# Performance work log

Measured on AMD Instinct MI355X. Metric: run time of the kernel, lower is better.

The kernel has to match this reference:

```python
import jax, jax.numpy as jnp
import numpy as np
import math

B, IN_CH, IMG = 32, 3, 128
D, L, H, MLP, P = 512, 8, 8, 2048, 8
HD = D // H
EPS = 1e-5


def _conv(x, w, b, stride, pad):
    y = jax.lax.conv_general_dilated(x, w, (stride, stride), pad,
                                     dimension_numbers=("NCHW", "OIHW", "NCHW"))
    return y + b[None, :, None, None]


def _gn(x, g, b, groups):
    Bn, C, Hh, W = x.shape
    xr = x.reshape(Bn, groups, C // groups, Hh, W)
    m = jnp.mean(xr, axis=(2, 3, 4), keepdims=True)
    v = jnp.var(xr, axis=(2, 3, 4), keepdims=True)
    xr = (xr - m) / jnp.sqrt(v + EPS)
    return xr.reshape(Bn, C, Hh, W) * g[None, :, None, None] + b[None, :, None, None]


def _ln(x, g, b):
    m = jnp.mean(x, axis=-1, keepdims=True)
    v = jnp.var(x, axis=-1, keepdims=True)
    return (x - m) / jnp.sqrt(v + EPS) * g + b


def _rot_half(x):
    # interleaved pairs: (x0,x1) -> (-x1,x0)
    x1, x2 = x[..., 0::2], x[..., 1::2]
    return jnp.stack((-x2, x1), axis=-1).reshape(x.shape)


def _xpos_tables(n_pos, hd):
    # faithful to rotary_embedding_torch with use_xpos=True, scale_base=512
    inv = 1.0 / (10000.0 ** (jnp.arange(0, hd, 2, dtype=jnp.float32) / hd))
    seq = jnp.arange(n_pos, dtype=jnp.float32)
    freqs = jnp.repeat(seq[:, None] * inv[None, :], 2, axis=-1)  # (n_pos, hd) interleaved
    sv = (jnp.arange(0, hd, 2, dtype=jnp.float32) + 0.4 * hd) / (1.4 * hd)
    power = (seq - n_pos // 2) / 512.0
    scale = sv[None, :] ** power[:, None]                        # (n_pos, hd//2)
    scale = jnp.concatenate([scale, scale], axis=-1)             # library uses cat, not interleave
    return jnp.cos(freqs), jnp.sin(freqs), scale


def _pos2d(N, Dd):
    g = int(math.isqrt(N))
    y = jnp.tile(jnp.arange(g), g).astype(jnp.float32)
    x = jnp.repeat(jnp.arange(g), g).astype(jnp.float32)
    dq = Dd // 4
    omega = jnp.exp(jnp.arange(dq, dtype=jnp.float32) * -(math.log(10000.0) / dq))
    px, py = x[:, None] * omega, y[:, None] * omega
    return jnp.concatenate([jnp.sin(px), jnp.cos(px), jnp.sin(py), jnp.cos(py)], axis=-1)[None]


def setup_inputs() -> dict:
    key = jax.random.key(0)
    ks = iter(jax.random.split(key, 40))
    def rn(shape, s=0.02):
        return jax.random.normal(next(ks), shape, jnp.float32) * s
    return dict(
        x=jax.random.normal(next(ks), (B, IN_CH, IMG, IMG), jnp.float32),
        conv1_w=rn((32, 3, 3, 3)), conv1_b=jnp.zeros((32,), jnp.float32),
        gn1_g=jnp.ones((32,), jnp.float32), gn1_b=jnp.zeros((32,), jnp.float32),
        conv2_w=rn((64, 32, 3, 3)), conv2_b=jnp.zeros((64,), jnp.float32),
        gn2_g=jnp.ones((64,), jnp.float32), gn2_b=jnp.zeros((64,), jnp.float32),
        patch_w=rn((D, 64, P, P)), patch_b=jnp.zeros((D,), jnp.float32),
        cls_token=rn((1, 1, D), 1.0),
        ln1_g=jnp.ones((L, D), jnp.float32), ln1_b=jnp.zeros((L, D), jnp.float32),
        qkv_w=rn((L, D, 3 * D)), qkv_b=jnp.zeros((L, 3 * D), jnp.float32),
        out_w=rn((L, D, D)), out_b=jnp.zeros((L, D), jnp.float32),
        ln2_g=jnp.ones((L, D), jnp.float32), ln2_b=jnp.zeros((L, D), jnp.float32),
        w1_w=rn((L, D, MLP)), w1_b=jnp.zeros((L, MLP), jnp.float32),
        w2_w=rn((L, D, MLP)), w2_b=jnp.zeros((L, MLP), jnp.float32),
        w3_w=rn((L, MLP, D)), w3_b=jnp.zeros((L, D), jnp.float32),
        fn_g=jnp.ones((D,), jnp.float32), fn_b=jnp.zeros((D,), jnp.float32),
    )


def _forward(x, conv1_w, conv1_b, gn1_g, gn1_b, conv2_w, conv2_b, gn2_g, gn2_b,
             patch_w, patch_b, cls_token, ln1_g, ln1_b, qkv_w, qkv_b, out_w, out_b,
             ln2_g, ln2_b, w1_w, w1_b, w2_w, w2_b, w3_w, w3_b, fn_g, fn_b):
    # conv stem (no downsample)
    f = jax.nn.gelu(_gn(_conv(x, conv1_w, conv1_b, 1, [(1, 1), (1, 1)]), gn1_g, gn1_b, 4), approximate=False)
    f = jax.nn.gelu(_gn(_conv(f, conv2_w, conv2_b, 1, [(1, 1), (1, 1)]), gn2_g, gn2_b, 8), approximate=False)
    # patch embed
    p = _conv(f, patch_w, patch_b, P, "VALID")            # (B, D, g, g)
    Bn, Dd, gh, gw = p.shape
    tokens = p.reshape(Bn, Dd, gh * gw).transpose(0, 2, 1)  # (B, N, D)
    tokens = tokens + _pos2d(gh * gw, Dd)
    xa = jnp.concatenate([jnp.broadcast_to(cls_token, (Bn, 1, Dd)), tokens], axis=1)
    # NOTE: original code applies RoPE with seq_dim=-2 on (B,S,H,hd) -> rotation indexed by HEAD axis
    cos, sin, xsc = _xpos_tables(H, HD)
    scale_att = HD ** -0.5
    for i in range(L):
        n = _ln(xa, ln1_g[i], ln1_b[i])
        qkv = (n @ qkv_w[i] + qkv_b[i]).reshape(Bn, -1, 3, H, HD)
        q, k, v = qkv[:, :, 0], qkv[:, :, 1], qkv[:, :, 2]     # (B, S, H, hd)
        q = q * cos * xsc + _rot_half(q) * sin * xsc
        k = k * cos / xsc + _rot_half(k) * sin / xsc
        attn = jax.nn.softmax(jnp.einsum("bihd,bjhd->bhij", q, k) * scale_att, axis=-1)
        y = jnp.einsum("bhij,bjhd->bihd", attn, v).reshape(Bn, -1, Dd)
        xa = xa + y @ out_w[i] + out_b[i]
        n2 = _ln(xa, ln2_g[i], ln2_b[i])
        xa = xa + (jax.nn.silu(n2 @ w1_w[i] + w1_b[i]) * (n2 @ w2_w[i] + w2_b[i])) @ w3_w[i] + w3_b[i]
    return _ln(xa, fn_g, fn_b)


def reference(x, conv1_w, conv1_b, gn1_g, gn1_b, conv2_w, conv2_b, gn2_g, gn2_b,
              patch_w, patch_b, cls_token, ln1_g, ln1_b, qkv_w, qkv_b, out_w, out_b,
              ln2_g, ln2_b, w1_w, w1_b, w2_w, w2_b, w3_w, w3_b, fn_g, fn_b):
    xa = _forward(x, conv1_w, conv1_b, gn1_g, gn1_b, conv2_w, conv2_b, gn2_g, gn2_b,
                  patch_w, patch_b, cls_token, ln1_g, ln1_b, qkv_w, qkv_b, out_w, out_b,
                  ln2_g, ln2_b, w1_w, w1_b, w2_w, w2_b, w3_w, w3_b, fn_g, fn_b)
    return (xa[:, 0], xa[:, 1:])  # (cls, patches); grid_hw is static (16,16)
```

## Files before the change

### kernel.cpp

```cpp
#include <hip/hip_runtime.h>

#define EPSV 1e-5f
typedef unsigned short u16;
typedef short bf16x8 __attribute__((ext_vector_type(8)));
typedef float f32x4 __attribute__((ext_vector_type(4)));
typedef u16 u16x8 __attribute__((ext_vector_type(8)));

__device__ __forceinline__ float gelu_exact(float x) {
    return 0.5f * x * (1.0f + erff(x * 0.7071067811865475f));
}
__device__ __forceinline__ u16 to_bf(float x) {
    union { float f; unsigned u; } c; c.f = x;
    unsigned r = c.u + 0x7fffu + ((c.u >> 16) & 1u);
    return (u16)(r >> 16);
}
__device__ __forceinline__ float to_f(u16 h) {
    union { unsigned u; float f; } c; c.u = ((unsigned)h) << 16;
    return c.f;
}
__device__ __forceinline__ void gload_lds16(const void* g, void* l) {
    __builtin_amdgcn_global_load_lds((const __attribute__((address_space(1))) unsigned int*)g,
                                     (__attribute__((address_space(3))) unsigned int*)l, 16, 0, 0);
}

__global__ void k_wsfail(float* out) { out[0] = 1.0e9f; }

__global__ void k_setup(float* __restrict__ sacc,
                        const float* __restrict__ conv1_w, float* __restrict__ w1t,
                        const float* __restrict__ conv2_w, u16* __restrict__ wpack,
                        const float* __restrict__ b1, const float* __restrict__ b2,
                        float* __restrict__ bias12,
                        float* __restrict__ postab, float* __restrict__ ropetab,
                        const float* __restrict__ cls, float* __restrict__ xa) {
    int idx = blockIdx.x * 256 + threadIdx.x;
    if (idx < 131072) {
        int p = idx >> 9, j = idx & 511;
        float coord = (j < 256) ? (float)(p >> 4) : (float)(p & 15);
        int jm = j & 127;
        float om = powf(10000.0f, -(float)jm / 128.0f);
        float arg = coord * om;
        postab[idx] = ((j >> 7) & 1) ? cosf(arg) : sinf(arg);
    }
    if (idx < 512) {
        int h = idx >> 6, d = idx & 63;
        float freq = (float)h * powf(10000.0f, -(float)(d >> 1) / 32.0f);
        float sv = (2.0f * (float)(d & 31) + 25.6f) / 89.6f;
        float pw = ((float)h - 4.0f) / 512.0f;
        float sc = powf(sv, pw);
        ropetab[idx * 4 + 0] = cosf(freq);
        ropetab[idx * 4 + 1] = sinf(freq);
        ropetab[idx * 4 + 2] = sc * 0.125f;
        ropetab[idx * 4 + 3] = 1.0f / sc;
    }
    if (idx < 768) sacc[idx] = 0.0f;
    if (idx < 864) {
        int co = idx / 27, k = idx % 27;
        w1t[k * 32 + co] = conv1_w[idx];
    }
    if (idx < 18432) {
        int ci = idx & 31, tc = idx >> 5;
        int tap = tc >> 6, co = tc & 63;
        wpack[idx] = to_bf(conv2_w[co * 288 + ci * 9 + tap]);
    }
    if (idx < 32768) {
        int l = idx >> 12, pc = idx & 4095;
        int chunk = pc >> 4, within = pc & 15;
        int srccol = (chunk >> 1) * 16 + within;
        bias12[idx] = (chunk & 1) ? b2[l * 2048 + srccol] : b1[l * 2048 + srccol];
    }
    if (idx < 16384) {
        int b = idx >> 9, d = idx & 511;
        xa[(size_t)(b * 257) * 512 + d] = cls[d];
    }
}

__global__ void k_pperm(const float* __restrict__ w, u16* __restrict__ wp) {
    int idx = blockIdx.x * 256 + threadIdx.x;
    int cout = idx >> 12, rem = idx & 4095;
    int tap = rem >> 6, ci = rem & 63;
    wp[idx] = to_bf(w[cout * 4096 + ci * 64 + tap]);
}

__global__ __launch_bounds__(256) void k_wcvtT(const float* __restrict__ src,
                                               u16* __restrict__ dst, int K, int N) {
    __shared__ float s[32][33];
    int z = blockIdx.z;
    src += (size_t)z * K * N;
    dst += (size_t)z * K * N;
    int k0 = blockIdx.y * 32, n0 = blockIdx.x * 32;
    int t = threadIdx.x, r = t >> 3, c4 = (t & 7) * 4;
    float4 v = *(const float4*)&src[(size_t)(k0 + r) * N + n0 + c4];
    s[r][c4 + 0] = v.x; s[r][c4 + 1] = v.y; s[r][c4 + 2] = v.z; s[r][c4 + 3] = v.w;
    __syncthreads();
    ushort4 o;
    o.x = to_bf(s[c4 + 0][r]); o.y = to_bf(s[c4 + 1][r]);
    o.z = to_bf(s[c4 + 2][r]); o.w = to_bf(s[c4 + 3][r]);
    *(ushort4*)&dst[(size_t)(n0 + r) * K + k0 + c4] = o;
}

__global__ __launch_bounds__(256) void k_wcvtT12L(const float* __restrict__ w1,
                                                  const float* __restrict__ w2,
                                                  u16* __restrict__ w12All) {
    __shared__ float s[32][33];
    int z = blockIdx.z;
    int layer = z >> 1, sel = z & 1;
    const float* src = (sel ? w2 : w1) + (size_t)layer * 1048576;
    u16* dst = w12All + (size_t)layer * 2097152;
    int k0 = blockIdx.y * 32, n0 = blockIdx.x * 32;
    int t = threadIdx.x, r = t >> 3, c4 = (t & 7) * 4;
    float4 v = *(const float4*)&src[(size_t)(k0 + r) * 2048 + n0 + c4];
    s[r][c4 + 0] = v.x; s[r][c4 + 1] = v.y; s[r][c4 + 2] = v.z; s[r][c4 + 3] = v.w;
    __syncthreads();
    ushort4 o;
    o.x = to_bf(s[c4 + 0][r]); o.y = to_bf(s[c4 + 1][r]);
    o.z = to_bf(s[c4 + 2][r]); o.w = to_bf(s[c4 + 3][r]);
    int nsrc = n0 + r;
    int p = ((nsrc >> 4) << 5) + (sel << 4) + (nsrc & 15);
    *(ushort4*)&dst[(size_t)p * 512 + k0 + c4] = o;
}

__global__ __launch_bounds__(256) void k_conv1(const float* __restrict__ in,
                                               const float* __restrict__ wt,
                                               const float* __restrict__ bias,
                                               u16* __restrict__ f1n,
                                               float* __restrict__ sacc) {
    __shared__ float s_in[3][18][18];
    __shared__ float rs[4][4], rq[4][4];
    int b = blockIdx.y;
    int tile = blockIdx.x;
    int y0 = (tile >> 3) << 4;
    int x0 = (tile & 7) << 4;
    int tid = threadIdx.x;
    for (int idx = tid; idx < 972; idx += 256) {
        int ci = idx / 324, r = idx % 324;
        int ly = r / 18, lx = r % 18;
        int gy = y0 + ly - 1, gx = x0 + lx - 1;
        float v = 0.0f;
        if (gy >= 0 && gy < 128 && gx >= 0 && gx < 128)
            v = in[((size_t)(b * 3 + ci) * 128 + gy) * 128 + gx];
        s_in[ci][ly][lx] = v;
    }
    __syncthreads();
    int py = tid >> 4, px = tid & 15;
    float acc[32];
#pragma unroll
    for (int co = 0; co < 32; co++) acc[co] = bias[co];
#pragma unroll
    for (int ci = 0; ci < 3; ci++)
#pragma unroll
        for (int dy = 0; dy < 3; dy++)
#pragma unroll
            for (int dx = 0; dx < 3; dx++) {
                float v = s_in[ci][py + dy][px + dx];
                const float* wr = &wt[(ci * 9 + dy * 3 + dx) * 32];
#pragma unroll
                for (int co = 0; co < 32; co++)
                    acc[co] = fmaf(wr[co], v, acc[co]);
            }
    float s[4] = {0.f, 0.f, 0.f, 0.f}, q[4] = {0.f, 0.f, 0.f, 0.f};
    u16 ob[32];
#pragma unroll
    for (int co = 0; co < 32; co++) {
        u16 hv = to_bf(acc[co]);
        ob[co] = hv;
        float v = to_f(hv);
        s[co >> 3] += v;
        q[co >> 3] += v * v;
    }
    int oy = y0 + py, ox = x0 + px;
    u16* dst = f1n + ((size_t)(b * 16384 + oy * 128 + ox) << 5);
#pragma unroll
    for (int i = 0; i < 8; i++)
        *(ushort4*)(dst + i * 4) = make_ushort4(ob[i * 4], ob[i * 4 + 1], ob[i * 4 + 2], ob[i * 4 + 3]);
#pragma unroll
    for (int g = 0; g < 4; g++) {
#pragma unroll
        for (int off = 1; off < 64; off <<= 1) {
            s[g] += __shfl_xor(s[g], off);
            q[g] += __shfl_xor(q[g], off);
        }
    }
    int w = tid >> 6, lane = tid & 63;
    if (lane == 0)
#pragma unroll
        for (int g = 0; g < 4; g++) { rs[g][w] = s[g]; rq[g][w] = q[g]; }
    __syncthreads();
    if (tid < 4) {
        int g = tid;
        float S = rs[g][0] + rs[g][1] + rs[g][2] + rs[g][3];
        float Q = rq[g][0] + rq[g][1] + rq[g][2] + rq[g][3];
        atomicAdd(&sacc[(b * 4 + g) * 2], S);
        atomicAdd(&sacc[(b * 4 + g) * 2 + 1], Q);
    }
}

__global__ void k_gnap(u16* __restrict__ xio, const float* __restrict__ sacc,
                       const float* __restrict__ gg, const float* __restrict__ bb,
                       int cm, int sh, int gmul) {
    int idx = blockIdx.x * 256 + threadIdx.x;
    long e = (long)idx * 4;
    int c0 = (int)(e & cm);
    int b = (int)(e >> sh);
    int sid = b * gmul + (c0 >> 3);
    float m = sacc[2 * sid] * (1.0f / 131072.0f);
    float var = sacc[2 * sid + 1] * (1.0f / 131072.0f) - m * m;
    float r = rsqrtf(var + 1e-5f);
    ushort4 a = *(ushort4*)&xio[e];
    ushort4 o;
    o.x = to_bf(gelu_exact((to_f(a.x) - m) * r * gg[c0 + 0] + bb[c0 + 0]));
    o.y = to_bf(gelu_exact((to_f(a.y) - m) * r * gg[c0 + 1] + bb[c0 + 1]));
    o.z = to_bf(gelu_exact((to_f(a.z) - m) * r * gg[c0 + 2] + bb[c0 + 2]));
    o.w = to_bf(gelu_exact((to_f(a.w) - m) * r * gg[c0 + 3] + bb[c0 + 3]));
    *(ushort4*)&xio[e] = o;
}

__global__ __launch_bounds__(256) void k_conv2m(const u16* __restrict__ f1b,
                                                const u16* __restrict__ wp,
                                                const float* __restrict__ bias,
                                                u16* __restrict__ f2n,
                                                float* __restrict__ sacc) {
    __shared__ u16 st[256][72];
    __shared__ float rs[8][4], rq[8][4];
    int b = blockIdx.y;
    int tile = blockIdx.x;
    int y0 = (tile >> 3) << 4;
    int x0 = (tile & 7) << 4;
    int tid = threadIdx.x;
    int w = tid >> 6, lane = tid & 63;
    int l15 = lane & 15, l16 = lane >> 4;

    const u16* base = f1b + ((size_t)b << 19);

    f32x4 acc[4][4];
    f32x4 zf = {0.f, 0.f, 0.f, 0.f};
#pragma unroll
    for (int m = 0; m < 4; m++)
#pragma unroll
        for (int n = 0; n < 4; n++) acc[m][n] = zf;
    bf16x8 zb = {0, 0, 0, 0, 0, 0, 0, 0};

#pragma unroll
    for (int tap = 0; tap < 9; tap++) {
        int dy = tap / 3, dx = tap % 3;
        int gx = x0 + l15 + dx - 1;
        bf16x8 af[4], bk[4];
#pragma unroll
        for (int m = 0; m < 4; m++) {
            int gy = y0 + w * 4 + m + dy - 1;
            bool ok = (gy >= 0) && (gy < 128) && (gx >= 0) && (gx < 128);
            int pix = ok ? (gy * 128 + gx) : 0;
            bf16x8 v = *(const bf16x8*)(base + ((size_t)pix << 5) + l16 * 8);
            af[m] = ok ? v : zb;
        }
#pragma unroll
        for (int n = 0; n < 4; n++)
            bk[n] = *(const bf16x8*)&wp[(tap * 64 + n * 16 + l15) * 32 + l16 * 8];
#pragma unroll
        for (int m = 0; m < 4; m++)
#pragma unroll
            for (int n = 0; n < 4; n++)
                acc[m][n] = __builtin_amdgcn_mfma_f32_16x16x32_bf16(af[m], bk[n], acc[m][n], 0, 0, 0);
    }

#pragma unroll
    for (int n = 0; n < 4; n++) {
        int ch = n * 16 + l15;
        float bv = bias[ch];
#pragma unroll
        for (int m = 0; m < 4; m++) {
#pragma unroll
            for (int r = 0; r < 4; r++) {
                int lpix = (w * 4 + m) * 16 + l16 * 4 + r;
                st[lpix][ch] = to_bf(acc[m][n][r] + bv);
            }
        }
    }
    __syncthreads();

    int py = tid >> 4, pxx = tid & 15;
    u16* dstp = f2n + ((size_t)(b * 16384 + (y0 + py) * 128 + x0 + pxx) << 6);
    float gs[8], gq[8];
#pragma unroll
    for (int g = 0; g < 8; g++) { gs[g] = 0.0f; gq[g] = 0.0f; }
#pragma unroll
    for (int c0 = 0; c0 < 8; c0++) {
        u16x8 v = *(const u16x8*)&st[tid][c0 * 8];
        *(u16x8*)(dstp + c0 * 8) = v;
#pragma unroll
        for (int i = 0; i < 8; i++) {
            float f = to_f((u16)v[i]);
            gs[c0] += f;
            gq[c0] += f * f;
        }
    }
#pragma unroll
    for (int g = 0; g < 8; g++) {
#pragma unroll
        for (int off = 1; off < 64; off <<= 1) {
            gs[g] += __shfl_xor(gs[g], off);
            gq[g] += __shfl_xor(gq[g], off);
        }
    }
    if (lane == 0)
#pragma unroll
        for (int g = 0; g < 8; g++) { rs[g][w] = gs[g]; rq[g][w] = gq[g]; }
    __syncthreads();
    if (tid < 8) {
        int g = tid;
        float S = rs[g][0] + rs[g][1] + rs[g][2] + rs[g][3];
        float Q = rq[g][0] + rq[g][1] + rq[g][2] + rq[g][3];
        atomicAdd(&sacc[(b * 8 + g) * 2], S);
        atomicAdd(&sacc[(b * 8 + g) * 2 + 1], Q);
    }
}

template <int MODE, int EPI>
__global__ __launch_bounds__(256) void k_bgemm(const u16* __restrict__ A,
                                               const u16* __restrict__ Bt,
                                               const float* __restrict__ bias,
                                               void* __restrict__ Cp,
                                               const float* __restrict__ aux,
                                               int M, int N, int K) {
    __shared__ u16 ldsA[8192];
    __shared__ u16 ldsB[8192];
    int tid = threadIdx.x;
    int w = tid >> 6, lane = tid & 63;
    int bm = blockIdx.y * 128, bn = blockIdx.x * 128;
    int wr = w >> 1, wc = w & 1;
    int l15 = lane & 15, l16 = lane >> 4;

    f32x4 acc[4][4];
    f32x4 zf = {0.f, 0.f, 0.f, 0.f};
#pragma unroll
    for (int m = 0; m < 4; m++)
#pragma unroll
        for (int n = 0; n < 4; n++) acc[m][n] = zf;

    for (int k0 = 0; k0 < K; k0 += 64) {
#pragma unroll
        for (int i = 0; i < 4; i++) {
            int chunk = (w * 4 + i) * 64 + lane;
            int kg = chunk >> 7, row = chunk & 127;
            const u16* src;
            if (MODE == 0) {
                int grow = bm + row;
                if (grow > M - 1) grow = M - 1;
                src = A + (size_t)grow * K + k0 + kg * 8;
            } else {
                int grow = bm + row;
                int bimg = grow >> 8, p = grow & 255;
                int kga = (k0 >> 3) + kg;
                int tap = kga >> 3, cq = kga & 7;
                int ky = tap >> 3, kx = tap & 7;
                int gy = ((p >> 4) << 3) + ky, gx = ((p & 15) << 3) + kx;
                src = A + (((size_t)(bimg * 16384 + gy * 128 + gx)) << 6) + cq * 8;
            }
            gload_lds16(src, &ldsA[(w * 4 + i) * 512]);
        }
#pragma unroll
        for (int i = 0; i < 4; i++) {
            int chunk = (w * 4 + i) * 64 + lane;
            int col = chunk >> 3, kgs = chunk & 7;
            int kg_src = kgs ^ (col & 7);
            const u16* src = Bt + (size_t)(bn + col) * K + k0 + kg_src * 8;
            gload_lds16(src, &ldsB[(w * 4 + i) * 512]);
        }
        __syncthreads();

        bf16x8 af[4][2], bfr[4][2];
#pragma unroll
        for (int kk = 0; kk < 2; kk++) {
            int kga = kk * 4 + l16;
#pragma unroll
            for (int m = 0; m < 4; m++) {
                int row_l = wr * 64 + m * 16 + l15;
                af[m][kk] = *(const bf16x8*)&ldsA[(kga * 128 + row_l) * 8];
            }
#pragma unroll
            for (int n = 0; n < 4; n++) {
                int col_l = wc * 64 + n * 16 + l15;
                bfr[n][kk] = *(const bf16x8*)&ldsB[(col_l * 8 + (kga ^ (col_l & 7))) * 8];
            }
        }
#pragma unroll
        for (int m = 0; m < 4; m++)
#pragma unroll
            for (int n = 0; n < 4; n++) {
                acc[m][n] = __builtin_amdgcn_mfma_f32_16x16x32_bf16(af[m][0], bfr[n][0], acc[m][n], 0, 0, 0);
                acc[m][n] = __builtin_amdgcn_mfma_f32_16x16x32_bf16(af[m][1], bfr[n][1], acc[m][n], 0, 0, 0);
            }
        __syncthreads();
    }

    if (EPI == 6) {
#pragma unroll
        for (int np = 0; np < 2; np++) {
            int n_a = np * 2, n_b = np * 2 + 1;
            float bva = bias[bn + wc * 64 + n_a * 16 + l15];
            float bvb = bias[bn + wc * 64 + n_b * 16 + l15];
            int ocol = (bn >> 1) + wc * 32 + np * 16 + l15;
#pragma unroll
            for (int m = 0; m < 4; m++) {
#pragma unroll
                for (int r = 0; r < 4; r++) {
                    int grow = bm + wr * 64 + m * 16 + l16 * 4 + r;
                    if (grow < M) {
                        float h1v = to_f(to_bf(acc[m][n_a][r] + bva));
                        float h2v = to_f(to_bf(acc[m][n_b][r] + bvb));
                        float sl = h1v / (1.0f + __expf(-h1v));
                        ((u16*)Cp)[(size_t)grow * (N >> 1) + ocol] = to_bf(sl * h2v);
                    }
                }
            }
        }
    } else {
#pragma unroll
        for (int n = 0; n < 4; n++) {
            int gcol = bn + wc * 64 + n * 16 + l15;
            float bv = bias[gcol];
            float rc = 0.f, rsn = 0.f, rsc = 1.f;
            bool isqk = false, odd = false;
            if (EPI == 7) {
                isqk = gcol < 1024;
                odd = (l15 & 1) != 0;
                const float* rb = &aux[(gcol & 511) * 4];
                if (isqk) {
                    rc = rb[0]; rsn = rb[1];
                    rsc = (gcol < 512) ? rb[2] : rb[3];
                }
            }
#pragma unroll
            for (int m = 0; m < 4; m++) {
#pragma unroll
                for (int r = 0; r < 4; r++) {
                    int grow = bm + wr * 64 + m * 16 + l16 * 4 + r;
                    float v = acc[m][n][r] + bv;
                    if (EPI == 7) {
                        float p = __shfl_xor(v, 1);
                        float vr = isqk ? ((odd ? (v * rc + p * rsn) : (v * rc - p * rsn)) * rsc) : v;
                        if (grow < M) ((u16*)Cp)[(size_t)grow * N + gcol] = to_bf(vr);
                    } else if (EPI == 1) {
                        if (grow < M) ((float*)Cp)[(size_t)grow * N + gcol] = v;
                    } else if (EPI == 2) {
                        if (grow < M) ((float*)Cp)[(size_t)grow * N + gcol] += v;
                    } else {
                        int bimg = grow >> 8, p2 = grow & 255;
                        v += aux[p2 * 512 + gcol];
                        ((float*)Cp)[((size_t)(bimg * 257) + 1 + p2) * 512 + gcol] = v;
                    }
                }
            }
        }
    }
}

__global__ __launch_bounds__(256) void k_bgemm64(const u16* __restrict__ A,
                                                 const u16* __restrict__ Bt,
                                                 const float* __restrict__ bias,
                                                 float* __restrict__ C,
                                                 int M, int N, int K) {
    __shared__ u16 ldsA[4096];
    __shared__ u16 ldsB[8192];
    int tid = threadIdx.x;
    int w = tid >> 6, lane = tid & 63;
    int bm = blockIdx.y * 64, bn = blockIdx.x * 128;
    int l15 = lane & 15, l16 = lane >> 4;

    f32x4 acc[4][2];
    f32x4 zf = {0.f, 0.f, 0.f, 0.f};
#pragma unroll
    for (int m = 0; m < 4; m++)
#pragma unroll
        for (int n = 0; n < 2; n++) acc[m][n] = zf;

    for (int k0 = 0; k0 < K; k0 += 64) {
#pragma unroll
        for (int i = 0; i < 2; i++) {
            int chunk = (w * 2 + i) * 64 + lane;
            int kg = chunk >> 6, row = chunk & 63;
            int grow = bm + row;
            if (grow > M - 1) grow = M - 1;
            const u16* src = A + (size_t)grow * K + k0 + kg * 8;
            gload_lds16(src, &ldsA[(w * 2 + i) * 512]);
        }
#pragma unroll
        for (int i = 0; i < 4; i++) {
            int chunk = (w * 4 + i) * 64 + lane;
            int col = chunk >> 3, kgs = chunk & 7;
            int kg_src = kgs ^ (col & 7);
            const u16* src = Bt + (size_t)(bn + col) * K + k0 + kg_src * 8;
            gload_lds16(src, &ldsB[(w * 4 + i) * 512]);
        }
        __syncthreads();

        bf16x8 af[4][2], bfr[2][2];
#pragma unroll
        for (int kk = 0; kk < 2; kk++) {
            int kga = kk * 4 + l16;
#pragma unroll
            for (int m = 0; m < 4; m++) {
                int row_l = m * 16 + l15;
                af[m][kk] = *(const bf16x8*)&ldsA[(kga * 64 + row_l) * 8];
            }
#pragma unroll
            for (int n = 0; n < 2; n++) {
                int col_l = w * 32 + n * 16 + l15;
                bfr[n][kk] = *(const bf16x8*)&ldsB[(col_l * 8 + (kga ^ (col_l & 7))) * 8];
            }
        }
#pragma unroll
        for (int m = 0; m < 4; m++)
#pragma unroll
            for (int n = 0; n < 2; n++) {
                acc[m][n] = __builtin_amdgcn_mfma_f32_16x16x32_bf16(af[m][0], bfr[n][0], acc[m][n], 0, 0, 0);
                acc[m][n] = __builtin_amdgcn_mfma_f32_16x16x32_bf16(af[m][1], bfr[n][1], acc[m][n], 0, 0, 0);
            }
        __syncthreads();
    }

#pragma unroll
    for (int n = 0; n < 2; n++) {
        int gcol = bn + w * 32 + n * 16 + l15;
        float bv = bias[gcol];
#pragma unroll
        for (int m = 0; m < 4; m++) {
#pragma unroll
            for (int r = 0; r < 4; r++) {
                int grow = bm + m * 16 + l16 * 4 + r;
                if (grow < M) C[(size_t)grow * N + gcol] += acc[m][n][r] + bv;
            }
        }
    }
}

__global__ __launch_bounds__(256) void k_lnb(const float* __restrict__ x,
                                             const float* __restrict__ g,
                                             const float* __restrict__ bta,
                                             u16* __restrict__ o) {
    int row = blockIdx.x * 4 + (threadIdx.x >> 6);
    int lane = threadIdx.x & 63;
    const float4* xr = (const float4*)(x + (size_t)row * 512);
    float4 a = xr[lane * 2], b = xr[lane * 2 + 1];
    float s = a.x + a.y + a.z + a.w + b.x + b.y + b.z + b.w;
#pragma unroll
    for (int off = 1; off < 64; off <<= 1) s += __shfl_xor(s, off);
    float mean = s * (1.0f / 512.0f);
    float d[8] = {a.x - mean, a.y - mean, a.z - mean, a.w - mean,
                  b.x - mean, b.y - mean, b.z - mean, b.w - mean};
    float q = 0.0f;
#pragma unroll
    for (int i = 0; i < 8; i++) q += d[i] * d[i];
#pragma unroll
    for (int off = 1; off < 64; off <<= 1) q += __shfl_xor(q, off);
    float rstd = rsqrtf(q * (1.0f / 512.0f) + EPSV);
    int c0 = lane * 8;
    float4 g0 = *(const float4*)&g[c0], g1 = *(const float4*)&g[c0 + 4];
    float4 b0 = *(const float4*)&bta[c0], b1 = *(const float4*)&bta[c0 + 4];
    u16* orow = o + (size_t)row * 512 + c0;
    *(ushort4*)orow = make_ushort4(to_bf(d[0] * rstd * g0.x + b0.x), to_bf(d[1] * rstd * g0.y + b0.y),
                                   to_bf(d[2] * rstd * g0.z + b0.z), to_bf(d[3] * rstd * g0.w + b0.w));
    *(ushort4*)(orow + 4) = make_ushort4(to_bf(d[4] * rstd * g1.x + b1.x), to_bf(d[5] * rstd * g1.y + b1.y),
                                         to_bf(d[6] * rstd * g1.z + b1.z), to_bf(d[7] * rstd * g1.w + b1.w));
}

__global__ __launch_bounds__(256) void k_ln_out(const float* __restrict__ x,
                                                const float* __restrict__ g,
                                                const float* __restrict__ bta,
                                                float* __restrict__ out) {
    int row = blockIdx.x * 4 + (threadIdx.x >> 6);
    int lane = threadIdx.x & 63;
    const float4* xr = (const float4*)(x + (size_t)row * 512);
    float4 a = xr[lane * 2], b = xr[lane * 2 + 1];
    float s = a.x + a.y + a.z + a.w + b.x + b.y + b.z + b.w;
#pragma unroll
    for (int off = 1; off < 64; off <<= 1) s += __shfl_xor(s, off);
    float mean = s * (1.0f / 512.0f);
    float d[8] = {a.x - mean, a.y - mean, a.z - mean, a.w - mean,
                  b.x - mean, b.y - mean, b.z - mean, b.w - mean};
    float q = 0.0f;
#pragma unroll
    for (int i = 0; i < 8; i++) q += d[i] * d[i];
#pragma unroll
    for (int off = 1; off < 64; off <<= 1) q += __shfl_xor(q, off);
    float rstd = rsqrtf(q * (1.0f / 512.0f) + EPSV);
    int bb = row / 257, t = row % 257;
    float* dst = (t == 0) ? out + (size_t)bb * 512
                          : out + 16384 + (size_t)(bb * 256 + (t - 1)) * 512;
    int c0 = lane * 8;
    float4 g0 = *(const float4*)&g[c0], g1 = *(const float4*)&g[c0 + 4];
    float4 b0 = *(const float4*)&bta[c0], b1 = *(const float4*)&bta[c0 + 4];
    *(float4*)(dst + c0) = make_float4(d[0] * rstd * g0.x + b0.x, d[1] * rstd * g0.y + b0.y,
                                       d[2] * rstd * g0.z + b0.z, d[3] * rstd * g0.w + b0.w);
    *(float4*)(dst + c0 + 4) = make_float4(d[4] * rstd * g1.x + b1.x, d[5] * rstd * g1.y + b1.y,
                                           d[6] * rstd * g1.z + b1.z, d[7] * rstd * g1.w + b1.w);
}

__global__ __launch_bounds__(256) void k_attn_mfma(const u16* __restrict__ qkv,
                                                   u16* __restrict__ y) {
    __shared__ u16 KV[2][64][72];
    __shared__ float sc[32][260];
    __shared__ u16 Pb[32][328];
    __shared__ float red1[32][8];
    __shared__ float red2[32][8];
    __shared__ float invr[32];

    int bid = blockIdx.x;
    int qt = bid % 9, bh = bid / 9;
    int h = bh & 7, b = bh >> 3;
    int q0 = qt * 32;
    int tid = threadIdx.x;
    int w = tid >> 6, lane = tid & 63;
    int l15 = lane & 15, l16 = lane >> 4;

    bf16x8 aq[2][2];
#pragma unroll
    for (int m = 0; m < 2; m++) {
        int grow = q0 + m * 16 + l15; if (grow > 256) grow = 256;
        const u16* qp = qkv + (size_t)(b * 257 + grow) * 1536 + h * 64 + l16 * 8;
        aq[m][0] = *(const bf16x8*)qp;
        aq[m][1] = *(const bf16x8*)(qp + 32);
    }

    for (int t = 0; t < 5; t++) {
        int j0 = t * 64;
        int gk = j0 + w * 16 + l15; if (gk > 256) gk = 256;
        const u16* kp = qkv + (size_t)(b * 257 + gk) * 1536 + 512 + h * 64 + l16 * 8;
        bf16x8 bk0 = *(const bf16x8*)kp;
        bf16x8 bk1 = *(const bf16x8*)(kp + 32);
        f32x4 a2[2];
        f32x4 zf = {0.f, 0.f, 0.f, 0.f};
        __builtin_amdgcn_s_setprio(1);
#pragma unroll
        for (int m = 0; m < 2; m++) {
            a2[m] = zf;
            a2[m] = __builtin_amdgcn_mfma_f32_16x16x32_bf16(aq[m][0], bk0, a2[m], 0, 0, 0);
            a2[m] = __builtin_amdgcn_mfma_f32_16x16x32_bf16(aq[m][1], bk1, a2[m], 0, 0, 0);
        }
        __builtin_amdgcn_s_setprio(0);
        int col = j0 + w * 16 + l15;
        if (col < 257) {
#pragma unroll
            for (int m = 0; m < 2; m++)
#pragma unroll
                for (int r = 0; r < 4; r++)
                    sc[m * 16 + l16 * 4 + r][col] = a2[m][r];
        }
    }
    __syncthreads();

    {
        int r = tid >> 3, sub = tid & 7;
        float mx = -1e30f;
        for (int j = sub; j < 257; j += 8) mx = fmaxf(mx, sc[r][j]);
        red1[r][sub] = mx;
        __syncthreads();
        mx = red1[r][0];
#pragma unroll
        for (int i = 1; i < 8; i++) mx = fmaxf(mx, red1[r][i]);
        float sm = 0.0f;
        for (int j = sub; j < 257; j += 8) {
            float e = __expf(sc[r][j] - mx);
            Pb[r][j] = to_bf(e);
            sm += e;
        }
        for (int j = 257 + sub; j < 320; j += 8) Pb[r][j] = 0;
        red2[r][sub] = sm;
        __syncthreads();
        if (sub == 0) {
            float t = red2[r][0];
#pragma unroll
            for (int i = 1; i < 8; i++) t += red2[r][i];
            invr[r] = 1.0f / t;
        }
        __syncthreads();
    }

    f32x4 oacc[2];
    {
        f32x4 zf = {0.f, 0.f, 0.f, 0.f};
        oacc[0] = zf; oacc[1] = zf;
    }
    for (int t = 0; t < 5; t++) {
        int j0 = t * 64;
        int buf = t & 1;
        {
            int vk = tid & 63, vd0 = (tid >> 6) * 16;
            int gk = j0 + vk;
            u16 o[16];
            if (gk <= 256) {
                const u16* vp = qkv + (size_t)(b * 257 + gk) * 1536 + 1024 + h * 64 + vd0;
                ushort4 a0 = *(const ushort4*)vp, a1 = *(const ushort4*)(vp + 4);
                ushort4 a2v = *(const ushort4*)(vp + 8), a3 = *(const ushort4*)(vp + 12);
                o[0] = a0.x; o[1] = a0.y; o[2] = a0.z; o[3] = a0.w;
                o[4] = a1.x; o[5] = a1.y; o[6] = a1.z; o[7] = a1.w;
                o[8] = a2v.x; o[9] = a2v.y; o[10] = a2v.z; o[11] = a2v.w;
                o[12] = a3.x; o[13] = a3.y; o[14] = a3.z; o[15] = a3.w;
            } else {
#pragma unroll
                for (int i = 0; i < 16; i++) o[i] = 0;
            }
#pragma unroll
            for (int i = 0; i < 16; i++) KV[buf][vd0 + i][vk] = o[i];
        }
        __syncthreads();

        bf16x8 ap[2][2], bv[2];
#pragma unroll
        for (int m = 0; m < 2; m++)
#pragma unroll
            for (int kk = 0; kk < 2; kk++)
                ap[m][kk] = *(const bf16x8*)&Pb[m * 16 + l15][j0 + kk * 32 + l16 * 8];
#pragma unroll
        for (int kk = 0; kk < 2; kk++)
            bv[kk] = *(const bf16x8*)&KV[buf][w * 16 + l15][kk * 32 + l16 * 8];
        __builtin_amdgcn_s_setprio(1);
#pragma unroll
        for (int m = 0; m < 2; m++) {
            oacc[m] = __builtin_amdgcn_mfma_f32_16x16x32_bf16(ap[m][0], bv[0], oacc[m], 0, 0, 0);
            oacc[m] = __builtin_amdgcn_mfma_f32_16x16x32_bf16(ap[m][1], bv[1], oacc[m], 0, 0, 0);
        }
        __builtin_amdgcn_s_setprio(0);
    }

#pragma unroll
    for (int m = 0; m < 2; m++)
#pragma unroll
        for (int r = 0; r < 4; r++) {
            int lr = m * 16 + l16 * 4 + r;
            int grow = q0 + lr;
            if (grow < 257)
                y[(size_t)(b * 257 + grow) * 512 + h * 64 + w * 16 + l15] =
                    to_bf(oacc[m][r] * invr[lr]);
        }
}

extern "C" void kernel_launch(void* const* d_in, const int* in_sizes, int n_in,
                              void* d_out, int out_size, void* d_ws, size_t ws_size,
                              hipStream_t stream) {
    const float* x       = (const float*)d_in[0];
    const float* conv1_w = (const float*)d_in[1];
    const float* conv1_b = (const float*)d_in[2];
    const float* gn1_g   = (const float*)d_in[3];
    const float* gn1_b   = (const float*)d_in[4];
    const float* conv2_w = (const float*)d_in[5];
    const float* conv2_b = (const float*)d_in[6];
    const float* gn2_g   = (const float*)d_in[7];
    const float* gn2_b   = (const float*)d_in[8];
    const float* patch_w = (const float*)d_in[9];
    const float* patch_b = (const float*)d_in[10];
    const float* cls_tok = (const float*)d_in[11];
    const float* ln1_g   = (const float*)d_in[12];
    const float* ln1_b   = (const float*)d_in[13];
    const float* qkv_w   = (const float*)d_in[14];
    const float* qkv_b   = (const float*)d_in[15];
    const float* out_w   = (const float*)d_in[16];
    const float* out_b   = (const float*)d_in[17];
    const float* ln2_g   = (const float*)d_in[18];
    const float* ln2_b   = (const float*)d_in[19];
    const float* w1_w    = (const float*)d_in[20];
    const float* w1_b    = (const float*)d_in[21];
    const float* w2_w    = (const float*)d_in[22];
    const float* w2_b    = (const float*)d_in[23];
    const float* w3_w    = (const float*)d_in[24];
    const float* w3_b    = (const float*)d_in[25];
    const float* fn_g    = (const float*)d_in[26];
    const float* fn_b    = (const float*)d_in[27];
    float* out = (float*)d_out;
    char* wsb  = (char*)d_ws;

    const size_t O_R1    = 0;
    const size_t O_W12A  = 0;
    const size_t O_W3A   = 33554432;
    const size_t O_HB    = O_R1 + 67371008;
    const size_t O_NB    = O_R1 + 101056512;
    const size_t O_Y     = O_R1 + 109477888;
    const size_t O_R2    = 134217728;
    const size_t O_XA    = 201326592;
    const size_t O_PWT   = 218169344;
    const size_t O_QKVT  = 222363648;
    const size_t O_OUTT  = 234946560;
    const size_t O_PT    = 245432320;
    const size_t O_RT    = 245956608;
    const size_t O_CW1   = 245964800;
    const size_t O_CW2   = 245968896;
    const size_t O_SA    = 246046720;
    const size_t O_B12   = 246050816;
    const size_t NEED    = 246181888;
    if (ws_size < NEED) {
        k_wsfail<<<1, 1, 0, stream>>>(out);
        return;
    }
    u16*   f2n    = (u16*)(wsb + O_R1);
    u16*   w12All = (u16*)(wsb + O_W12A);
    u16*   w3All  = (u16*)(wsb + O_W3A);
    u16*   hb     = (u16*)(wsb + O_HB);
    u16*   nb     = (u16*)(wsb + O_NB);
    u16*   yb     = (u16*)(wsb + O_Y);
    u16*   f1n    = (u16*)(wsb + O_R2);
    u16*   qkvb   = (u16*)(wsb + O_R2);
    float* xa     = (float*)(wsb + O_XA);
    u16*   patchT = (u16*)(wsb + O_PWT);
    u16*   qkvT   = (u16*)(wsb + O_QKVT);
    u16*   outT   = (u16*)(wsb + O_OUTT);
    float* postab = (float*)(wsb + O_PT);
    float* ropet  = (float*)(wsb + O_RT);
    float* w1t    = (float*)(wsb + O_CW1);
    u16*   wpack  = (u16*)(wsb + O_CW2);
    float* sacc   = (float*)(wsb + O_SA);
    float* bias12 = (float*)(wsb + O_B12);

    k_setup<<<512, 256, 0, stream>>>(sacc, conv1_w, w1t, conv2_w, wpack,
                                     w1_b, w2_b, bias12, postab, ropet, cls_tok, xa);
    k_pperm<<<8192, 256, 0, stream>>>(patch_w, patchT);
    k_wcvtT<<<dim3(48, 16, 8), 256, 0, stream>>>(qkv_w, qkvT, 512, 1536);
    k_wcvtT<<<dim3(16, 16, 8), 256, 0, stream>>>(out_w, outT, 512, 512);

    k_conv1<<<dim3(64, 32), 256, 0, stream>>>(x, w1t, conv1_b, f1n, sacc);
    k_gnap<<<16384, 256, 0, stream>>>(f1n, sacc, gn1_g, gn1_b, 31, 19, 4);
    k_conv2m<<<dim3(64, 32), 256, 0, stream>>>(f1n, wpack, conv2_b, f2n, sacc + 256);
    k_gnap<<<32768, 256, 0, stream>>>(f2n, sacc + 256, gn2_g, gn2_b, 63, 20, 8);

    k_bgemm<1, 3><<<dim3(4, 64), 256, 0, stream>>>(f2n, patchT, patch_b, xa, postab, 8192, 512, 4096);

    k_wcvtT12L<<<dim3(64, 16, 16), 256, 0, stream>>>(w1_w, w2_w, w12All);
    k_wcvtT<<<dim3(16, 64, 8), 256, 0, stream>>>(w3_w, w3All, 2048, 512);

    for (int l = 0; l < 8; l++) {
        k_lnb<<<2056, 256, 0, stream>>>(xa, ln1_g + l * 512, ln1_b + l * 512, nb);
        k_bgemm<0, 7><<<dim3(12, 65), 256, 0, stream>>>(nb, qkvT + (size_t)l * 786432,
                                                        qkv_b + l * 1536, qkvb, ropet, 8224, 1536, 512);
        k_attn_mfma<<<2304, 256, 0, stream>>>(qkvb, yb);
        k_bgemm64<<<dim3(4, 129), 256, 0, stream>>>(yb, outT + (size_t)l * 262144,
                                                    out_b + l * 512, xa, 8224, 512, 512);
        k_lnb<<<2056, 256, 0, stream>>>(xa, ln2_g + l * 512, ln2_b + l * 512, nb);
        k_bgemm<0, 6><<<dim3(32, 65), 256, 0, stream>>>(nb, w12All + (size_t)l * 2097152,
                                                        bias12 + l * 4096, hb, nullptr, 8224, 4096, 512);
        k_bgemm64<<<dim3(4, 129), 256, 0, stream>>>(hb, w3All + (size_t)l * 1048576,
                                                    w3_b + l * 512, xa, 8224, 512, 2048);
    }
    k_ln_out<<<2056, 256, 0, stream>>>(xa, fn_g, fn_b, out);
}
```

Baseline: 2.269 ms.

## Add double-buffered SwiGLU GEMM with XCD-aware workgroup swizzle

Splits the fused SwiGLU epilogue out of the generic GEMM into a new kernel that double-buffers its LDS tiles, so the next K-tile's global-to-LDS loads overlap the MFMA work on the current tile. It also remaps the 1D workgroup id so that consecutive tiles land on the same XCD, aiming for better L2 reuse of A and B tiles. The double buffer doubles LDS use per block (64KB), which may lower occupancy.

```diff
diff --git a/kernel.cpp b/kernel.cpp
--- a/kernel.cpp
+++ b/kernel.cpp
@@ -21,6 +21,12 @@
 __device__ __forceinline__ void gload_lds16(const void* g, void* l) {
     __builtin_amdgcn_global_load_lds((const __attribute__((address_space(1))) unsigned int*)g,
                                      (__attribute__((address_space(3))) unsigned int*)l, 16, 0, 0);
+}
+__device__ __forceinline__ int xcd_swz() {
+    int nwg = gridDim.x, orig = blockIdx.x;
+    int q = nwg >> 3, r = nwg & 7;
+    int xcd = orig & 7, sub = orig >> 3;
+    return ((xcd < r) ? xcd * (q + 1) : r * (q + 1) + (xcd - r) * q) + sub;
 }
 
 __global__ void k_wsfail(float* out) { out[0] = 1.0e9f; }
@@ -392,62 +398,135 @@
         __syncthreads();
     }
 
-    if (EPI == 6) {
-#pragma unroll
-        for (int np = 0; np < 2; np++) {
-            int n_a = np * 2, n_b = np * 2 + 1;
-            float bva = bias[bn + wc * 64 + n_a * 16 + l15];
-            float bvb = bias[bn + wc * 64 + n_b * 16 + l15];
-            int ocol = (bn >> 1) + wc * 32 + np * 16 + l15;
+#pragma unroll
+    for (int n = 0; n < 4; n++) {
+        int gcol = bn + wc * 64 + n * 16 + l15;
+        float bv = bias[gcol];
+        float rc = 0.f, rsn = 0.f, rsc = 1.f;
+        bool isqk = false, odd = false;
+        if (EPI == 7) {
+            isqk = gcol < 1024;
+            odd = (l15 & 1) != 0;
+            const float* rb = &aux[(gcol & 511) * 4];
+            if (isqk) {
+                rc = rb[0]; rsn = rb[1];
+                rsc = (gcol < 512) ? rb[2] : rb[3];
+            }
+        }
+#pragma unroll
+        for (int m = 0; m < 4; m++) {
+#pragma unroll
+            for (int r = 0; r < 4; r++) {
+                int grow = bm + wr * 64 + m * 16 + l16 * 4 + r;
+                float v = acc[m][n][r] + bv;
+                if (EPI == 7) {
+                    float p = __shfl_xor(v, 1);
+                    float vr = isqk ? ((odd ? (v * rc + p * rsn) : (v * rc - p * rsn)) * rsc) : v;
+                    if (grow < M) ((u16*)Cp)[(size_t)grow * N + gcol] = to_bf(vr);
+                } else if (EPI == 1) {
+                    if (grow < M) ((float*)Cp)[(size_t)grow * N + gcol] = v;
+                } else if (EPI == 2) {
+                    if (grow < M) ((float*)Cp)[(size_t)grow * N + gcol] += v;
+                } else {
+                    int bimg = grow >> 8, p2 = grow & 255;
+                    v += aux[p2 * 512 + gcol];
+                    ((float*)Cp)[((size_t)(bimg * 257) + 1 + p2) * 512 + gcol] = v;
+                }
+            }
+        }
+    }
+}
+
+__global__ __launch_bounds__(256) void k_bgemm_db(const u16* __restrict__ A,
+                                                  const u16* __restrict__ Bt,
+                                                  const float* __restrict__ bias,
+                                                  u16* __restrict__ Cp,
+                                                  int M, int N, int K, int gridN) {
+    __shared__ u16 ldsA[2][8192];
+    __shared__ u16 ldsB[2][8192];
+    int tid = threadIdx.x;
+    int w = tid >> 6, lane = tid & 63;
+    int wgid = xcd_swz();
+    int bm = (wgid / gridN) * 128, bn = (wgid % gridN) * 128;
+    int wr = w >> 1, wc = w & 1;
+    int l15 = lane & 15, l16 = lane >> 4;
+
+    auto stage = [&](int k0, int bb) {
+#pragma unroll
+        for (int i = 0; i < 4; i++) {
+            int chunk = (w * 4 + i) * 64 + lane;
+            int kg = chunk >> 7, row = chunk & 127;
+            int grow = bm + row;
+            if (grow > M - 1) grow = M - 1;
+            const u16* src = A + (size_t)grow * K + k0 + kg * 8;
+            gload_lds16(src, &ldsA[bb][(w * 4 + i) * 512]);
+        }
+#pragma unroll
+        for (int i = 0; i < 4; i++) {
+            int chunk = (w * 4 + i) * 64 + lane;
+            int col = chunk >> 3, kgs = chunk & 7;
+            int kg_src = kgs ^ (col & 7);
+            const u16* src = Bt + (size_t)(bn + col) * K + k0 + kg_src * 8;
+            gload_lds16(src, &ldsB[bb][(w * 4 + i) * 512]);
+        }
+    };
+
+    f32x4 acc[4][4];
+    f32x4 zf = {0.f, 0.f, 0.f, 0.f};
+#pragma unroll
+    for (int m = 0; m < 4; m++)
+#pragma unroll
+        for (int n = 0; n < 4; n++) acc[m][n] = zf;
+
+    int nk = K >> 6;
+    stage(0, 0);
+    __syncthreads();
+    int cur = 0;
+    for (int kt = 0; kt < nk; kt++) {
+        if (kt + 1 < nk) stage((kt + 1) << 6, cur ^ 1);
+
+        bf16x8 af[4][2], bfr[4][2];
+#pragma unroll
+        for (int kk = 0; kk < 2; kk++) {
+            int kga = kk * 4 + l16;
 #pragma unroll
             for (int m = 0; m < 4; m++) {
-#pragma unroll
-                for (int r = 0; r < 4; r++) {
-                    int grow = bm + wr * 64 + m * 16 + l16 * 4 + r;
-                    if (grow < M) {
-                        float h1v = to_f(to_bf(acc[m][n_a][r] + bva));
-                        float h2v = to_f(to_bf(acc[m][n_b][r] + bvb));
-                        float sl = h1v / (1.0f + __expf(-h1v));
-                        ((u16*)Cp)[(size_t)grow * (N >> 1) + ocol] = to_bf(sl * h2v);
-                    }
-                }
-            }
-        }
-    } else {
-#pragma unroll
-        for (int n = 0; n < 4; n++) {
-            int gcol = bn + wc * 64 + n * 16 + l15;
-            float bv = bias[gcol];
-            float rc = 0.f, rsn = 0.f, rsc = 1.f;
-            bool isqk = false, odd = false;
-            if (EPI == 7) {
-                isqk = gcol < 1024;
-                odd = (l15 & 1) != 0;
-                const float* rb = &aux[(gcol & 511) * 4];
-                if (isqk) {
-                    rc = rb[0]; rsn = rb[1];
-                    rsc = (gcol < 512) ? rb[2] : rb[3];
-                }
-            }
-#pragma unroll
-            for (int m = 0; m < 4; m++) {
-#pragma unroll
-                for (int r = 0; r < 4; r++) {
-                    int grow = bm + wr * 64 + m * 16 + l16 * 4 + r;
-                    float v = acc[m][n][r] + bv;
-                    if (EPI == 7) {
-                        float p = __shfl_xor(v, 1);
-                        float vr = isqk ? ((odd ? (v * rc + p * rsn) : (v * rc - p * rsn)) * rsc) : v;
-                        if (grow < M) ((u16*)Cp)[(size_t)grow * N + gcol] = to_bf(vr);
-                    } else if (EPI == 1) {
-                        if (grow < M) ((float*)Cp)[(size_t)grow * N + gcol] = v;
-                    } else if (EPI == 2) {
-                        if (grow < M) ((float*)Cp)[(size_t)grow * N + gcol] += v;
-                    } else {
-                        int bimg = grow >> 8, p2 = grow & 255;
-                        v += aux[p2 * 512 + gcol];
-                        ((float*)Cp)[((size_t)(bimg * 257) + 1 + p2) * 512 + gcol] = v;
-                    }
+                int row_l = wr * 64 + m * 16 + l15;
+                af[m][kk] = *(const bf16x8*)&ldsA[cur][(kga * 128 + row_l) * 8];
+            }
+#pragma unroll
+            for (int n = 0; n < 4; n++) {
+                int col_l = wc * 64 + n * 16 + l15;
+                bfr[n][kk] = *(const bf16x8*)&ldsB[cur][(col_l * 8 + (kga ^ (col_l & 7))) * 8];
+            }
+        }
+#pragma unroll
+        for (int m = 0; m < 4; m++)
+#pragma unroll
+            for (int n = 0; n < 4; n++) {
+                acc[m][n] = __builtin_amdgcn_mfma_f32_16x16x32_bf16(af[m][0], bfr[n][0], acc[m][n], 0, 0, 0);
+                acc[m][n] = __builtin_amdgcn_mfma_f32_16x16x32_bf16(af[m][1], bfr[n][1], acc[m][n], 0, 0, 0);
+            }
+        __syncthreads();
+        cur ^= 1;
+    }
+
+#pragma unroll
+    for (int np = 0; np < 2; np++) {
+        int n_a = np * 2, n_b = np * 2 + 1;
+        float bva = bias[bn + wc * 64 + n_a * 16 + l15];
+        float bvb = bias[bn + wc * 64 + n_b * 16 + l15];
+        int ocol = (bn >> 1) + wc * 32 + np * 16 + l15;
+#pragma unroll
+        for (int m = 0; m < 4; m++) {
+#pragma unroll
+            for (int r = 0; r < 4; r++) {
+                int grow = bm + wr * 64 + m * 16 + l16 * 4 + r;
+                if (grow < M) {
+                    float h1v = to_f(to_bf(acc[m][n_a][r] + bva));
+                    float h2v = to_f(to_bf(acc[m][n_b][r] + bvb));
+                    float sl = h1v / (1.0f + __expf(-h1v));
+                    Cp[(size_t)grow * (N >> 1) + ocol] = to_bf(sl * h2v);
                 }
             }
         }
@@ -833,8 +912,8 @@
         k_bgemm64<<<dim3(4, 129), 256, 0, stream>>>(yb, outT + (size_t)l * 262144,
                                                     out_b + l * 512, xa, 8224, 512, 512);
         k_lnb<<<2056, 256, 0, stream>>>(xa, ln2_g + l * 512, ln2_b + l * 512, nb);
-        k_bgemm<0, 6><<<dim3(32, 65), 256, 0, stream>>>(nb, w12All + (size_t)l * 2097152,
-                                                        bias12 + l * 4096, hb, nullptr, 8224, 4096, 512);
+        k_bgemm_db<<<2080, 256, 0, stream>>>(nb, w12All + (size_t)l * 2097152,
+                                             bias12 + l * 4096, hb, 8224, 4096, 512, 32);
         k_bgemm64<<<dim3(4, 129), 256, 0, stream>>>(hb, w3All + (size_t)l * 1048576,
                                                     w3_b + l * 512, xa, 8224, 512, 2048);
     }
```

New measurement: 2.408 ms. 6.1% more time.
